# Performance work log

Hardware: AMD Instinct MI355X
Metric: run time of the kernel (lower is better)

The kernel has to match this reference:

```python
import jax, jax.numpy as jnp
import numpy as np

N = 50000   # nodes
E = 800000  # edges
F = 16      # raw feature width (sliced 4:10 -> 6)
H = 256     # hidden_dim
O = 128     # out_dim
NE = 4      # n_experts
G = 64      # graphs in batch
K = 2       # top_k
XS, XE = 4, 10
SPS = 0.3   # size_prior_strength


def setup_inputs() -> dict:
    key = jax.random.key(0)
    ks = jax.random.split(key, 16)
    rn = lambda k, s: jax.random.normal(k, s, dtype=jnp.float32) * 0.05
    return dict(
        x=jax.random.normal(ks[0], (N, F), dtype=jnp.float32),
        edge_index=jax.random.randint(ks[1], (2, E), 0, N),
        batch=jnp.sort(jax.random.randint(ks[2], (N,), 0, G)),
        enc_W1=rn(ks[3], (6, H)), enc_b1=jnp.zeros(H, jnp.float32),
        enc_W2=rn(ks[4], (H, H)), enc_b2=jnp.zeros(H, jnp.float32),
        r_W1=rn(ks[5], (H + 3, H)), r_b1=jnp.zeros(H, jnp.float32),
        ln_g=jnp.ones(H, jnp.float32), ln_b=jnp.zeros(H, jnp.float32),
        r_W2=rn(ks[6], (H, NE)), r_b2=jnp.zeros(NE, jnp.float32),
        size_centers=jnp.linspace(0.0, 1.0, NE, dtype=jnp.float32),
        W0_rel=rn(ks[7], (NE, H, H)), b0_rel=jnp.zeros((NE, H), jnp.float32), W0_root=rn(ks[8], (NE, H, H)),
        W1_rel=rn(ks[9], (NE, H, H)), b1_rel=jnp.zeros((NE, H), jnp.float32), W1_root=rn(ks[10], (NE, H, H)),
        W2_rel=rn(ks[11], (NE, H, O)), b2_rel=jnp.zeros((NE, O), jnp.float32), W2_root=rn(ks[12], (NE, H, O)),
    )


def _forward(x, edge_index, batch, enc_W1, enc_b1, enc_W2, enc_b2,
             r_W1, r_b1, ln_g, ln_b, r_W2, r_b2, size_centers,
             W0_rel, b0_rel, W0_root, W1_rel, b1_rel, W1_root, W2_rel, b2_rel, W2_root):
    src, dst = edge_index[0], edge_index[1]
    xs = x[:, XS:XE]                                   # [N,6]
    h = jax.nn.relu(xs @ enc_W1 + enc_b1) @ enc_W2 + enc_b2  # [N,H]

    # per-graph size features (bincounts via scatter-add)
    n = jnp.maximum(jnp.zeros(G, jnp.float32).at[batch].add(1.0), 1.0)
    e = jnp.zeros(G, jnp.float32).at[batch[src]].add(1.0)
    density = e / jnp.maximum(n * (n - 1.0), 1.0)
    logn = jnp.log(n)
    logn_norm = (logn - logn.min()) / (logn.max() - logn.min() + 1e-6)
    feats = jnp.stack([n, e, density], -1)             # [G,3]
    feats = (feats - feats.mean(0, keepdims=True)) / (feats.std(0, keepdims=True) + 1e-6)
    sf = feats[batch]                                   # [N,3]
    ln_node = logn_norm[batch]                          # [N]

    # router: Linear -> LayerNorm -> ReLU -> Linear, combined with size prior
    inp = jnp.concatenate([h, sf], -1)                  # [N,H+3]
    t = inp @ r_W1 + r_b1
    t = (t - t.mean(-1, keepdims=True)) * jax.lax.rsqrt(t.var(-1, keepdims=True) + 1e-5) * ln_g + ln_b
    learned = jax.nn.relu(t) @ r_W2 + r_b2              # [N,NE]
    prior = -(ln_node[:, None] - size_centers[None, :]) ** 2
    logits = (1.0 - SPS) * learned + SPS * prior        # temperature = 1.0

    # top-k gate
    probs = jax.nn.softmax(logits, -1)
    top_vals, top_idx = jax.lax.top_k(probs, K)
    top_vals = top_vals / (top_vals.sum(-1, keepdims=True) + 1e-8)
    weights = jnp.zeros_like(probs).at[jnp.arange(N)[:, None], top_idx].set(top_vals)

    # GraphConv experts: out = lin_rel(sum_{j->i} x_j) + lin_root(x_i)
    def aggregate(v):  # [N,C] -> [N,C] scatter-add of src features onto dst
        return jnp.zeros_like(v).at[dst].add(v[src])

    agg_h = aggregate(h)
    hE = jax.nn.relu(jnp.einsum('nh,eho->eno', agg_h, W0_rel) + b0_rel[:, None, :]
                     + jnp.einsum('nh,eho->eno', h, W0_root))            # [NE,N,H]
    aggE = jax.vmap(aggregate)(hE)
    hE = jax.nn.relu(jnp.einsum('enh,eho->eno', aggE, W1_rel) + b1_rel[:, None, :]
                     + jnp.einsum('enh,eho->eno', hE, W1_root))          # [NE,N,H]
    aggE = jax.vmap(aggregate)(hE)
    outE = (jnp.einsum('enh,eho->eno', aggE, W2_rel) + b2_rel[:, None, :]
            + jnp.einsum('enh,eho->eno', hE, W2_root))                   # [NE,N,O]

    return jnp.einsum('eno,ne->no', outE, weights)                       # [N,O]


def reference(x, edge_index, batch, enc_W1, enc_b1, enc_W2, enc_b2,
              r_W1, r_b1, ln_g, ln_b, r_W2, r_b2, size_centers,
              W0_rel, b0_rel, W0_root, W1_rel, b1_rel, W1_root, W2_rel, b2_rel, W2_root):
    return _forward(x, edge_index, batch, enc_W1, enc_b1, enc_W2, enc_b2,
                    r_W1, r_b1, ln_g, ln_b, r_W2, r_b2, size_centers,
                    W0_rel, b0_rel, W0_root, W1_rel, b1_rel, W1_root, W2_rel, b2_rel, W2_root)
```

## Files before the change

kernel.cpp:

```cpp
#include <hip/hip_runtime.h>
#include <hip/hip_bf16.h>

#define H_DIM 256
#define O_DIM 128
#define NEXP 4
#define G_DIM 64

typedef unsigned short ushort_t;
typedef unsigned int uint_t;
typedef __attribute__((ext_vector_type(8))) short short8;
typedef __attribute__((ext_vector_type(4))) float floatx4;

__device__ __forceinline__ float bf2f(ushort_t u) {
    union { uint_t i; float f; } c; c.i = ((uint_t)u) << 16; return c.f;
}
__device__ __forceinline__ ushort_t f2bf(float f) {
    union { float f; uint_t i; } c; c.f = f;
    uint_t x = c.i;
    uint_t r = (x + 0x7fffu + ((x >> 16) & 1u)) >> 16;
    return (ushort_t)r;
}

__device__ __forceinline__ void load16_lds(const void* g, void* l) {
    __builtin_amdgcn_global_load_lds(
        (const __attribute__((address_space(1))) unsigned int*)g,
        (__attribute__((address_space(3))) unsigned int*)l, 16, 0, 0);
}

__global__ void zero_i_kernel(int* __restrict__ p, long n) {
    long i = (long)blockIdx.x * blockDim.x + threadIdx.x;
    if (i < n) p[i] = 0;
}

__global__ void wsplit2_kernel(const float* __restrict__ Wa, const float* __restrict__ Wb,
                               ushort_t* __restrict__ Wh) {
    int z = blockIdx.y;
    int i = blockIdx.x * 256 + threadIdx.x;
    if (i >= 131072) return;
    int nn = i >> 9, kk = i & 511;
    float v = (kk < 256) ? Wa[(long)z * 65536 + kk * 256 + nn]
                         : Wb[(long)z * 65536 + (kk - 256) * 256 + nn];
    Wh[(long)z * 131072 + i] = f2bf(v);
}

__global__ void wsplitcat_kernel(const float* __restrict__ Wa, const float* __restrict__ Wb,
                                 ushort_t* __restrict__ Wh) {
    int z = blockIdx.y;
    int i = blockIdx.x * 256 + threadIdx.x;
    if (i >= 65536) return;
    int nn = i >> 8, kk = i & 255;
    float v = (nn < 128) ? Wa[(long)z * 32768 + kk * 128 + nn]
                         : Wb[(long)z * 32768 + kk * 128 + (nn - 128)];
    Wh[(long)z * 65536 + i] = f2bf(v);
}

__global__ void encoder1_kernel(const float* __restrict__ x, const float* __restrict__ W1,
                                const float* __restrict__ b1, float* __restrict__ u,
                                int N, int F) {
    int n = blockIdx.x;
    int j = threadIdx.x;
    float acc = b1[j];
    #pragma unroll
    for (int c = 0; c < 6; ++c)
        acc += x[(long)n * F + 4 + c] * W1[c * H_DIM + j];
    u[(long)n * H_DIM + j] = fmaxf(acc, 0.f);
}

__global__ __launch_bounds__(256)
void gemm256_kernel(const float* __restrict__ A, const float* __restrict__ W,
                    const float* __restrict__ bias, float* __restrict__ C,
                    ushort_t* __restrict__ Cbf, int M, int Nc) {
    const int K = 256;
    __shared__ float As[16][68];
    __shared__ float Ws[16][68];
    int tid = threadIdx.x;
    int tx = tid & 15, ty = tid >> 4;
    int row0 = blockIdx.x * 64;
    int col0 = blockIdx.y * 64;
    float acc[4][4] = {};
    int lrow = tid >> 2, kq = tid & 3;
    int wk = tid >> 4, wc = (tid & 15) * 4;
    for (int k0 = 0; k0 < K; k0 += 16) {
        float4 av = make_float4(0.f, 0.f, 0.f, 0.f);
        int arow = row0 + lrow;
        if (arow < M) av = *(const float4*)(A + (long)arow * K + k0 + kq * 4);
        As[kq * 4 + 0][lrow] = av.x;
        As[kq * 4 + 1][lrow] = av.y;
        As[kq * 4 + 2][lrow] = av.z;
        As[kq * 4 + 3][lrow] = av.w;
        float4 wv = *(const float4*)(W + (long)(k0 + wk) * Nc + col0 + wc);
        *(float4*)&Ws[wk][wc] = wv;
        __syncthreads();
        #pragma unroll
        for (int kk = 0; kk < 16; ++kk) {
            float a[4], b[4];
            #pragma unroll
            for (int i = 0; i < 4; ++i) a[i] = As[kk][ty * 4 + i];
            #pragma unroll
            for (int j = 0; j < 4; ++j) b[j] = Ws[kk][tx * 4 + j];
            #pragma unroll
            for (int i = 0; i < 4; ++i)
                #pragma unroll
                for (int j = 0; j < 4; ++j) acc[i][j] += a[i] * b[j];
        }
        __syncthreads();
    }
    #pragma unroll
    for (int i = 0; i < 4; ++i) {
        int r = row0 + ty * 4 + i;
        if (r >= M) break;
        #pragma unroll
        for (int j = 0; j < 4; ++j) {
            int c = col0 + tx * 4 + j;
            float v = acc[i][j];
            if (bias) v += bias[c];
            C[(long)r * Nc + c] = v;
            if (Cbf) Cbf[(long)r * Nc + c] = f2bf(v);
        }
    }
}

template<int NH>
__global__ __launch_bounds__(256)
void gemm_bf_kernel(const ushort_t* __restrict__ A1, long sA1z, int rsA1,
                    const ushort_t* __restrict__ A2, long sA2z, int rsA2,
                    const ushort_t* __restrict__ B, long sBz,
                    const float* __restrict__ bias, int sBiasz,
                    ushort_t* __restrict__ Cbf, long sCz, int rsC,
                    int M, int Kb, int relu) {
    __shared__ alignas(16) ushort_t Asl[2][64 * 32];
    __shared__ alignas(16) ushort_t Bsl[2][128 * 32];

    const int tid = threadIdx.x, wave = tid >> 6, lane = tid & 63;
    const int z = blockIdx.z;
    const int row0 = blockIdx.x * 64, col0 = blockIdx.y * 128;
    const int wr = (wave >> 1) * 32, wcx = (wave & 1) * 64;
    floatx4 acc[2][4] = {};

    A1 += (long)z * sA1z;
    A2 += (long)z * sA2z;
    B += (long)z * sBz;
    if (bias) bias += (long)z * sBiasz;
    Cbf += (long)z * sCz;

    const int bsr = lane >> 2;
    const int bgc = ((lane & 3) - (bsr >> 1)) & 3;
    long aoff1, aoff2;
    {
        int ar = row0 + wave * 16 + bsr;
        ar = ar < M ? ar : M - 1;
        aoff1 = (long)ar * rsA1 + bgc * 8;
        aoff2 = (long)ar * rsA2 + bgc * 8;
    }
    const long brow = (long)(col0 + wave * 32 + bsr) * Kb + bgc * 8;
    const ushort_t* Bg0 = B + brow;
    const ushort_t* Bg1 = B + brow + (long)16 * Kb;
    const int laA  = (wave * 16) * 32;
    const int laB0 = (wave * 32) * 32;
    const int laB1 = (wave * 32 + 16) * 32;

    const int fm = lane & 15, fq = lane >> 4;
    const int NK = NH * 8;

    load16_lds(A1 + aoff1, &Asl[0][laA]);
    load16_lds(Bg0, &Bsl[0][laB0]);
    load16_lds(Bg1, &Bsl[0][laB1]);
    __syncthreads();

    for (int k = 0; k < NK; ++k) {
        const int buf = k & 1;
        short8 a[2], b[4];
        #pragma unroll
        for (int j = 0; j < 4; ++j) {
            int row = wcx + j * 16 + fm;
            int slot = (fq + ((row >> 1) & 3)) & 3;
            b[j] = *(const short8*)&Bsl[buf][row * 32 + slot * 8];
        }
        #pragma unroll
        for (int i = 0; i < 2; ++i) {
            int row = wr + i * 16 + fm;
            int slot = (fq + ((row >> 1) & 3)) & 3;
            a[i] = *(const short8*)&Asl[buf][row * 32 + slot * 8];
        }
        if (k + 1 < NK) {
            const int kn = k + 1, bn = kn & 1;
            const ushort_t* Ab = (kn >> 3) ? A2 : A1;
            const long ao = (kn >> 3) ? aoff2 : aoff1;
            const int k0 = (kn & 7) * 32;
            const int kk = kn * 32;
            load16_lds(Ab + ao + k0, &Asl[bn][laA]);
            load16_lds(Bg0 + kk, &Bsl[bn][laB0]);
            load16_lds(Bg1 + kk, &Bsl[bn][laB1]);
        }
        #pragma unroll
        for (int i = 0; i < 2; ++i)
            #pragma unroll
            for (int j = 0; j < 4; ++j)
                acc[i][j] = __builtin_amdgcn_mfma_f32_16x16x32_bf16(a[i], b[j], acc[i][j], 0, 0, 0);
        if (k + 1 < NK) __syncthreads();
    }

    #pragma unroll
    for (int i = 0; i < 2; ++i) {
        #pragma unroll
        for (int j = 0; j < 4; ++j) {
            int col = col0 + wcx + j * 16 + fm;
            int rowb = row0 + wr + i * 16 + fq * 4;
            #pragma unroll
            for (int r = 0; r < 4; ++r) {
                int row = rowb + r;
                if (row < M) {
                    float v = acc[i][j][r];
                    if (bias) v += bias[col];
                    if (relu) v = fmaxf(v, 0.f);
                    Cbf[(long)row * rsC + col] = f2bf(v);
                }
            }
        }
    }
}

__global__ void hist_nodes_kernel(const int* __restrict__ batch, int n, int* __restrict__ gn) {
    __shared__ int bins[G_DIM];
    int t = threadIdx.x;
    if (t < G_DIM) bins[t] = 0;
    __syncthreads();
    for (long i = (long)blockIdx.x * blockDim.x + t; i < n; i += (long)gridDim.x * blockDim.x)
        atomicAdd(&bins[batch[i]], 1);
    __syncthreads();
    if (t < G_DIM) atomicAdd(&gn[t], bins[t]);
}

__global__ void hist_edges_kernel(const int* __restrict__ ei, const int* __restrict__ batch,
                                  int E, int* __restrict__ ge) {
    __shared__ int bins[G_DIM];
    int t = threadIdx.x;
    if (t < G_DIM) bins[t] = 0;
    __syncthreads();
    for (long i = (long)blockIdx.x * blockDim.x + t; i < E; i += (long)gridDim.x * blockDim.x)
        atomicAdd(&bins[batch[ei[i]]], 1);
    __syncthreads();
    if (t < G_DIM) atomicAdd(&ge[t], bins[t]);
}

__global__ void graph_stats_kernel(const int* __restrict__ gn, const int* __restrict__ ge,
                                   float* __restrict__ feats_norm, float* __restrict__ logn_norm) {
    int g = threadIdx.x;
    float nv = fmaxf((float)gn[g], 1.0f);
    float ev = (float)ge[g];
    float density = ev / fmaxf(nv * (nv - 1.0f), 1.0f);
    float logn = logf(nv);
    float mn = logn, mx = logn;
    for (int o = 32; o; o >>= 1) {
        mn = fminf(mn, __shfl_xor(mn, o));
        mx = fmaxf(mx, __shfl_xor(mx, o));
    }
    logn_norm[g] = (logn - mn) / (mx - mn + 1e-6f);
    float f[3] = {nv, ev, density};
    #pragma unroll
    for (int c = 0; c < 3; ++c) {
        float s = f[c];
        for (int o = 32; o; o >>= 1) s += __shfl_xor(s, o);
        float mean = s / 64.f;
        float d = f[c] - mean;
        float v = d * d;
        for (int o = 32; o; o >>= 1) v += __shfl_xor(v, o);
        float stdv = sqrtf(v / 64.f);
        feats_norm[g * 3 + c] = d / (stdv + 1e-6f);
    }
}

__global__ __launch_bounds__(256)
void router_epi_kernel(const float* __restrict__ t, const int* __restrict__ batch,
                       const float* __restrict__ feats_norm, const float* __restrict__ logn_norm,
                       const float* __restrict__ rW1, const float* __restrict__ rb1,
                       const float* __restrict__ lng, const float* __restrict__ lnb,
                       const float* __restrict__ rW2, const float* __restrict__ rb2,
                       const float* __restrict__ centers, float* __restrict__ w, int N) {
    int wave = threadIdx.x >> 6, lane = threadIdx.x & 63;
    int n = blockIdx.x * 4 + wave;
    if (n >= N) return;
    int g = batch[n];
    float sf0 = feats_norm[g * 3 + 0], sf1 = feats_norm[g * 3 + 1], sf2 = feats_norm[g * 3 + 2];
    float ln = logn_norm[g];
    float tv[4];
    #pragma unroll
    for (int q = 0; q < 4; ++q) {
        int j = lane + 64 * q;
        tv[q] = t[(long)n * H_DIM + j] + rb1[j]
              + sf0 * rW1[256 * H_DIM + j] + sf1 * rW1[257 * H_DIM + j] + sf2 * rW1[258 * H_DIM + j];
    }
    float s = tv[0] + tv[1] + tv[2] + tv[3];
    for (int o = 32; o; o >>= 1) s += __shfl_xor(s, o);
    float mean = s / 256.f;
    float vs = 0.f;
    #pragma unroll
    for (int q = 0; q < 4; ++q) { float d = tv[q] - mean; vs += d * d; }
    for (int o = 32; o; o >>= 1) vs += __shfl_xor(vs, o);
    float rstd = rsqrtf(vs / 256.f + 1e-5f);
    float le[NEXP] = {0.f, 0.f, 0.f, 0.f};
    #pragma unroll
    for (int q = 0; q < 4; ++q) {
        int j = lane + 64 * q;
        float y = (tv[q] - mean) * rstd * lng[j] + lnb[j];
        y = fmaxf(y, 0.f);
        #pragma unroll
        for (int e = 0; e < NEXP; ++e) le[e] += y * rW2[j * NEXP + e];
    }
    #pragma unroll
    for (int e = 0; e < NEXP; ++e)
        for (int o = 32; o; o >>= 1) le[e] += __shfl_xor(le[e], o);
    if (lane == 0) {
        float p[NEXP];
        float m = -1e30f;
        #pragma unroll
        for (int e = 0; e < NEXP; ++e) {
            float d = ln - centers[e];
            float lv = 0.7f * (le[e] + rb2[e]) + 0.3f * (-(d * d));
            p[e] = lv;
            m = fmaxf(m, lv);
        }
        float ssum = 0.f;
        #pragma unroll
        for (int e = 0; e < NEXP; ++e) { p[e] = expf(p[e] - m); ssum += p[e]; }
        #pragma unroll
        for (int e = 0; e < NEXP; ++e) p[e] /= ssum;
        int i1 = 0;
        for (int e = 1; e < NEXP; ++e) if (p[e] > p[i1]) i1 = e;
        int i2 = -1;
        for (int e = 0; e < NEXP; ++e) { if (e == i1) continue; if (i2 < 0 || p[e] > p[i2]) i2 = e; }
        float denom = p[i1] + p[i2] + 1e-8f;
        float out4[NEXP] = {0.f, 0.f, 0.f, 0.f};
        out4[i1] = p[i1] / denom;
        out4[i2] = p[i2] / denom;
        #pragma unroll
        for (int e = 0; e < NEXP; ++e) w[(long)n * NEXP + e] = out4[e];
    }
}

__global__ void count_dst_kernel(const int* __restrict__ ei, int E, int* __restrict__ cnt) {
    int i = blockIdx.x * blockDim.x + threadIdx.x;
    if (i < E) atomicAdd(&cnt[ei[E + i]], 1);
}

__global__ __launch_bounds__(1024)
void scan_kernel(const int* __restrict__ cnt, int* __restrict__ row_ptr, int n) {
    __shared__ int buf[1024];
    __shared__ int carry_s;
    int tid = threadIdx.x;
    if (tid == 0) carry_s = 0;
    __syncthreads();
    for (int base = 0; base < n; base += 1024) {
        int v = (base + tid < n) ? cnt[base + tid] : 0;
        buf[tid] = v;
        __syncthreads();
        for (int off = 1; off < 1024; off <<= 1) {
            int tv = (tid >= off) ? buf[tid - off] : 0;
            __syncthreads();
            buf[tid] += tv;
            __syncthreads();
        }
        int carry = carry_s;
        if (base + tid < n) row_ptr[base + tid] = carry + buf[tid] - v;
        __syncthreads();
        if (tid == 1023) carry_s = carry + buf[1023];
        __syncthreads();
    }
    if (tid == 0) row_ptr[n] = carry_s;
}

__global__ void fill_csr_kernel(const int* __restrict__ ei, int E, const int* __restrict__ row_ptr,
                                int* __restrict__ fillc, int* __restrict__ srcs) {
    int i = blockIdx.x * blockDim.x + threadIdx.x;
    if (i < E) {
        int d = ei[E + i];
        int pos = row_ptr[d] + atomicAdd(&fillc[d], 1);
        srcs[pos] = ei[i];
    }
}

__global__ __launch_bounds__(256)
void agg_b2b_kernel(const ushort_t* __restrict__ feat, ushort_t* __restrict__ outp,
                    const int* __restrict__ rp, const int* __restrict__ srcs, int N) {
    int wave = threadIdx.x >> 6, lane = threadIdx.x & 63;
    int n = blockIdx.x * 4 + wave;
    if (n >= N) return;
    float a0 = 0.f, a1 = 0.f, a2 = 0.f, a3 = 0.f;
    int p0 = rp[n], p1 = rp[n + 1];
    const ushort_t* base = feat + lane * 4;
    int p = p0;
    for (; p + 3 < p1; p += 4) {
        uint2 v0 = *(const uint2*)(base + (long)srcs[p] * H_DIM);
        uint2 v1 = *(const uint2*)(base + (long)srcs[p + 1] * H_DIM);
        uint2 v2 = *(const uint2*)(base + (long)srcs[p + 2] * H_DIM);
        uint2 v3 = *(const uint2*)(base + (long)srcs[p + 3] * H_DIM);
        a0 += bf2f((ushort_t)(v0.x & 0xffff)) + bf2f((ushort_t)(v1.x & 0xffff))
            + bf2f((ushort_t)(v2.x & 0xffff)) + bf2f((ushort_t)(v3.x & 0xffff));
        a1 += bf2f((ushort_t)(v0.x >> 16)) + bf2f((ushort_t)(v1.x >> 16))
            + bf2f((ushort_t)(v2.x >> 16)) + bf2f((ushort_t)(v3.x >> 16));
        a2 += bf2f((ushort_t)(v0.y & 0xffff)) + bf2f((ushort_t)(v1.y & 0xffff))
            + bf2f((ushort_t)(v2.y & 0xffff)) + bf2f((ushort_t)(v3.y & 0xffff));
        a3 += bf2f((ushort_t)(v0.y >> 16)) + bf2f((ushort_t)(v1.y >> 16))
            + bf2f((ushort_t)(v2.y >> 16)) + bf2f((ushort_t)(v3.y >> 16));
    }
    for (; p < p1; ++p) {
        uint2 v = *(const uint2*)(base + (long)srcs[p] * H_DIM);
        a0 += bf2f((ushort_t)(v.x & 0xffff));
        a1 += bf2f((ushort_t)(v.x >> 16));
        a2 += bf2f((ushort_t)(v.y & 0xffff));
        a3 += bf2f((ushort_t)(v.y >> 16));
    }
    uint2 o;
    o.x = (uint_t)f2bf(a0) | ((uint_t)f2bf(a1) << 16);
    o.y = (uint_t)f2bf(a2) | ((uint_t)f2bf(a3) << 16);
    *(uint2*)(outp + (long)n * H_DIM + lane * 4) = o;
}

__global__ void aggI_kernel(const ushort_t* __restrict__ feat, ushort_t* __restrict__ outp,
                            const int* __restrict__ rp, const int* __restrict__ srcs,
                            int N, int W) {
    int n = blockIdx.x;
    int t = threadIdx.x;
    float a[8] = {0.f, 0.f, 0.f, 0.f, 0.f, 0.f, 0.f, 0.f};
    int p0 = rp[n], p1 = rp[n + 1];
    const ushort_t* base = feat + t * 8;
    int p = p0;
    for (; p + 3 < p1; p += 4) {
        uint4 v0 = *(const uint4*)(base + (long)srcs[p] * W);
        uint4 v1 = *(const uint4*)(base + (long)srcs[p + 1] * W);
        uint4 v2 = *(const uint4*)(base + (long)srcs[p + 2] * W);
        uint4 v3 = *(const uint4*)(base + (long)srcs[p + 3] * W);
        uint_t w0[4] = {v0.x, v0.y, v0.z, v0.w};
        uint_t w1[4] = {v1.x, v1.y, v1.z, v1.w};
        uint_t w2[4] = {v2.x, v2.y, v2.z, v2.w};
        uint_t w3[4] = {v3.x, v3.y, v3.z, v3.w};
        #pragma unroll
        for (int q = 0; q < 4; ++q) {
            a[2 * q]     += bf2f((ushort_t)(w0[q] & 0xffff)) + bf2f((ushort_t)(w1[q] & 0xffff))
                          + bf2f((ushort_t)(w2[q] & 0xffff)) + bf2f((ushort_t)(w3[q] & 0xffff));
            a[2 * q + 1] += bf2f((ushort_t)(w0[q] >> 16)) + bf2f((ushort_t)(w1[q] >> 16))
                          + bf2f((ushort_t)(w2[q] >> 16)) + bf2f((ushort_t)(w3[q] >> 16));
        }
    }
    for (; p < p1; ++p) {
        uint4 v = *(const uint4*)(base + (long)srcs[p] * W);
        uint_t w[4] = {v.x, v.y, v.z, v.w};
        #pragma unroll
        for (int q = 0; q < 4; ++q) {
            a[2 * q]     += bf2f((ushort_t)(w[q] & 0xffff));
            a[2 * q + 1] += bf2f((ushort_t)(w[q] >> 16));
        }
    }
    uint4 o;
    o.x = (uint_t)f2bf(a[0]) | ((uint_t)f2bf(a[1]) << 16);
    o.y = (uint_t)f2bf(a[2]) | ((uint_t)f2bf(a[3]) << 16);
    o.z = (uint_t)f2bf(a[4]) | ((uint_t)f2bf(a[5]) << 16);
    o.w = (uint_t)f2bf(a[6]) | ((uint_t)f2bf(a[7]) << 16);
    *(uint4*)(outp + (long)n * W + t * 8) = o;
}

__global__ __launch_bounds__(256)
void final_mixE_kernel(const ushort_t* __restrict__ PR, const float* __restrict__ b2,
                       const float* __restrict__ wts, int e0, int EB,
                       const int* __restrict__ rp, const int* __restrict__ srcs,
                       float* __restrict__ out, int N, int init) {
    int wave = threadIdx.x >> 6, lane = threadIdx.x & 63;
    int n = blockIdx.x * 4 + wave;
    if (n >= N) return;
    const int W = EB * 256;
    int c0 = lane * 2;
    long obase = (long)n * O_DIM + c0;
    float o0 = init ? 0.f : out[obase];
    float o1 = init ? 0.f : out[obase + 1];
    int zs[2]; float wv[2]; int na = 0;
    for (int z = 0; z < EB; ++z) {
        float w = wts[(long)n * NEXP + e0 + z];
        if (w != 0.f && na < 2) { zs[na] = z; wv[na] = w; ++na; }
    }
    if (na) {
        const ushort_t* P0 = PR + zs[0] * 256 + c0;
        const ushort_t* P1 = PR + zs[na - 1] * 256 + c0;
        float a00 = 0.f, a01 = 0.f, a10 = 0.f, a11 = 0.f;
        int p0 = rp[n], p1 = rp[n + 1];
        if (na == 2) {
            int p = p0;
            for (; p + 1 < p1; p += 2) {
                long s0 = (long)srcs[p] * W;
                long s1 = (long)srcs[p + 1] * W;
                uint_t v00 = *(const uint_t*)(P0 + s0);
                uint_t v10 = *(const uint_t*)(P1 + s0);
                uint_t v01 = *(const uint_t*)(P0 + s1);
                uint_t v11 = *(const uint_t*)(P1 + s1);
                a00 += bf2f((ushort_t)(v00 & 0xffff)) + bf2f((ushort_t)(v01 & 0xffff));
                a01 += bf2f((ushort_t)(v00 >> 16))    + bf2f((ushort_t)(v01 >> 16));
                a10 += bf2f((ushort_t)(v10 & 0xffff)) + bf2f((ushort_t)(v11 & 0xffff));
                a11 += bf2f((ushort_t)(v10 >> 16))    + bf2f((ushort_t)(v11 >> 16));
            }
            if (p < p1) {
                long s = (long)srcs[p] * W;
                uint_t v0 = *(const uint_t*)(P0 + s);
                uint_t v1 = *(const uint_t*)(P1 + s);
                a00 += bf2f((ushort_t)(v0 & 0xffff)); a01 += bf2f((ushort_t)(v0 >> 16));
                a10 += bf2f((ushort_t)(v1 & 0xffff)); a11 += bf2f((ushort_t)(v1 >> 16));
            }
        } else {
            int p = p0;
            for (; p + 3 < p1; p += 4) {
                uint_t v0 = *(const uint_t*)(P0 + (long)srcs[p] * W);
                uint_t v1 = *(const uint_t*)(P0 + (long)srcs[p + 1] * W);
                uint_t v2 = *(const uint_t*)(P0 + (long)srcs[p + 2] * W);
                uint_t v3 = *(const uint_t*)(P0 + (long)srcs[p + 3] * W);
                a00 += bf2f((ushort_t)(v0 & 0xffff)) + bf2f((ushort_t)(v1 & 0xffff))
                     + bf2f((ushort_t)(v2 & 0xffff)) + bf2f((ushort_t)(v3 & 0xffff));
                a01 += bf2f((ushort_t)(v0 >> 16)) + bf2f((ushort_t)(v1 >> 16))
                     + bf2f((ushort_t)(v2 >> 16)) + bf2f((ushort_t)(v3 >> 16));
            }
            for (; p < p1; ++p) {
                uint_t v = *(const uint_t*)(P0 + (long)srcs[p] * W);
                a00 += bf2f((ushort_t)(v & 0xffff)); a01 += bf2f((ushort_t)(v >> 16));
            }
        }
        {
            int e = e0 + zs[0];
            uint_t rv = *(const uint_t*)(PR + (long)n * W + zs[0] * 256 + 128 + c0);
            o0 += wv[0] * (a00 + bf2f((ushort_t)(rv & 0xffff)) + b2[e * O_DIM + c0]);
            o1 += wv[0] * (a01 + bf2f((ushort_t)(rv >> 16))    + b2[e * O_DIM + c0 + 1]);
        }
        if (na == 2) {
            int e = e0 + zs[1];
            uint_t rv = *(const uint_t*)(PR + (long)n * W + zs[1] * 256 + 128 + c0);
            o0 += wv[1] * (a10 + bf2f((ushort_t)(rv & 0xffff)) + b2[e * O_DIM + c0]);
            o1 += wv[1] * (a11 + bf2f((ushort_t)(rv >> 16))    + b2[e * O_DIM + c0 + 1]);
        }
    }
    out[obase] = o0;
    out[obase + 1] = o1;
}

extern "C" void kernel_launch(void* const* d_in, const int* in_sizes, int n_in,
                              void* d_out, int out_size, void* d_ws, size_t ws_size,
                              hipStream_t stream) {
    const float* x       = (const float*)d_in[0];
    const int*   ei      = (const int*)  d_in[1];
    const int*   batch   = (const int*)  d_in[2];
    const float* enc_W1  = (const float*)d_in[3];
    const float* enc_b1  = (const float*)d_in[4];
    const float* enc_W2  = (const float*)d_in[5];
    const float* enc_b2  = (const float*)d_in[6];
    const float* r_W1    = (const float*)d_in[7];
    const float* r_b1    = (const float*)d_in[8];
    const float* ln_g    = (const float*)d_in[9];
    const float* ln_b    = (const float*)d_in[10];
    const float* r_W2    = (const float*)d_in[11];
    const float* r_b2    = (const float*)d_in[12];
    const float* centers = (const float*)d_in[13];
    const float* W0_rel  = (const float*)d_in[14];
    const float* b0_rel  = (const float*)d_in[15];
    const float* W0_root = (const float*)d_in[16];
    const float* W1_rel  = (const float*)d_in[17];
    const float* b1_rel  = (const float*)d_in[18];
    const float* W1_root = (const float*)d_in[19];
    const float* W2_rel  = (const float*)d_in[20];
    const float* b2_rel  = (const float*)d_in[21];
    const float* W2_root = (const float*)d_in[22];

    const int N = in_sizes[2];
    const int E = in_sizes[1] / 2;
    const int F = in_sizes[0] / N;

    char* ws = (char*)d_ws;
    size_t off = 0;
    auto alloc = [&](size_t bytes) -> void* {
        void* p = ws + off;
        off += (bytes + 255) & ~(size_t)255;
        return p;
    };
    int* cnt      = (int*)alloc((size_t)N * 4);
    int* fillc    = (int*)alloc((size_t)N * 4);
    int* gn       = (int*)alloc((size_t)G_DIM * 4);
    int* ge       = (int*)alloc((size_t)G_DIM * 4);
    size_t zero_bytes = off;
    int* row_ptr  = (int*)alloc((size_t)(N + 1) * 4);
    int* srcs     = (int*)alloc((size_t)E * 4);
    float* feats_norm = (float*)alloc((size_t)G_DIM * 3 * 4);
    float* logn_norm  = (float*)alloc((size_t)G_DIM * 4);
    float* wts    = (float*)alloc((size_t)N * NEXP * 4);
    ushort_t* wf0  = (ushort_t*)alloc((size_t)NEXP * 131072 * 2);
    ushort_t* wf1  = (ushort_t*)alloc((size_t)NEXP * 131072 * 2);
    ushort_t* wfin = (ushort_t*)alloc((size_t)NEXP * 65536 * 2);

    const long sE = (long)N * H_DIM;
    size_t fixed_end = off;
    size_t slab4 = ((size_t)4 * sE * 2 + 255) & ~(size_t)255;
    size_t slab2 = ((size_t)2 * sE * 2 + 255) & ~(size_t)255;
    size_t need4 = fixed_end + 3 * slab4 + (1u << 20);

    int EB;
    ushort_t *S1, *S2, *S3, *h_bf, *aggh_bf;
    float *u, *h, *tf32;
    if (ws_size >= need4) {
        EB = 4;
        S1 = (ushort_t*)alloc(slab4);
        S2 = (ushort_t*)alloc(slab4);
        S3 = (ushort_t*)alloc(slab4);
        u = (float*)S1; h = (float*)S2;
        h_bf = S3; aggh_bf = S3 + sE;
        tf32 = (float*)(S3 + 2 * sE);
    } else {
        EB = 2;
        h_bf    = (ushort_t*)alloc((size_t)sE * 2);
        aggh_bf = (ushort_t*)alloc((size_t)sE * 2);
        S1 = (ushort_t*)alloc(slab2);
        S2 = (ushort_t*)alloc(slab2);
        S3 = (ushort_t*)alloc(slab2);
        u = (float*)S1; h = (float*)S2; tf32 = (float*)S3;
    }
    (void)out_size; (void)n_in;

    ushort_t* hE0  = S1;
    ushort_t* aggE = S2;
    ushort_t* hE1  = S3;
    ushort_t* PR   = S1;
    float* out = (float*)d_out;

    const int W  = EB * 256;
    dim3 blk256(256);
    dim3 gR((N + 63) / 64, H_DIM / 64, 1);
    dim3 gM((N + 63) / 64, 2, EB);
    dim3 gAgg((N + 3) / 4);

    {
        long nz = (long)(zero_bytes / 4);
        zero_i_kernel<<<dim3((nz + 255) / 256), blk256, 0, stream>>>((int*)ws, nz);
    }
    wsplit2_kernel<<<dim3(512, NEXP), blk256, 0, stream>>>(W0_rel, W0_root, wf0);
    wsplit2_kernel<<<dim3(512, NEXP), blk256, 0, stream>>>(W1_rel, W1_root, wf1);
    wsplitcat_kernel<<<dim3(256, NEXP), blk256, 0, stream>>>(W2_rel, W2_root, wfin);
    encoder1_kernel<<<dim3(N), blk256, 0, stream>>>(x, enc_W1, enc_b1, u, N, F);
    gemm256_kernel<<<gR, blk256, 0, stream>>>(u, enc_W2, enc_b2, h, h_bf, N, H_DIM);
    hist_nodes_kernel<<<dim3(256), blk256, 0, stream>>>(batch, N, gn);
    hist_edges_kernel<<<dim3(512), blk256, 0, stream>>>(ei, batch, E, ge);
    graph_stats_kernel<<<dim3(1), dim3(64), 0, stream>>>(gn, ge, feats_norm, logn_norm);
    gemm256_kernel<<<gR, blk256, 0, stream>>>(h, r_W1, nullptr, tf32, nullptr, N, H_DIM);
    router_epi_kernel<<<dim3((N + 3) / 4), blk256, 0, stream>>>(
        tf32, batch, feats_norm, logn_norm, r_W1, r_b1, ln_g, ln_b, r_W2, r_b2, centers, wts, N);
    count_dst_kernel<<<dim3((E + 255) / 256), blk256, 0, stream>>>(ei, E, cnt);
    scan_kernel<<<dim3(1), dim3(1024), 0, stream>>>(cnt, row_ptr, N);
    fill_csr_kernel<<<dim3((E + 255) / 256), blk256, 0, stream>>>(ei, E, row_ptr, fillc, srcs);
    agg_b2b_kernel<<<gAgg, blk256, 0, stream>>>(h_bf, aggh_bf, row_ptr, srcs, N);

    for (int b = 0; b < NEXP / EB; ++b) {
        const int e0 = b * EB;
        gemm_bf_kernel<2><<<gM, blk256, 0, stream>>>(
            aggh_bf, 0, 256, h_bf, 0, 256,
            wf0 + (long)e0 * 131072, 131072,
            b0_rel + e0 * H_DIM, H_DIM, hE0, 256, W, N, 512, 1);
        aggI_kernel<<<dim3(N), dim3(W / 8), 0, stream>>>(hE0, aggE, row_ptr, srcs, N, W);
        gemm_bf_kernel<2><<<gM, blk256, 0, stream>>>(
            aggE, 256, W, hE0, 256, W,
            wf1 + (long)e0 * 131072, 131072,
            b1_rel + e0 * H_DIM, H_DIM, hE1, 256, W, N, 512, 1);
        gemm_bf_kernel<1><<<gM, blk256, 0, stream>>>(
            hE1, 256, W, nullptr, 0, 256,
            wfin + (long)e0 * 65536, 65536,
            nullptr, 0, PR, 256, W, N, 256, 0);
        final_mixE_kernel<<<gAgg, blk256, 0, stream>>>(
            PR, b2_rel, wts, e0, EB, row_ptr, srcs, out, N, b == 0 ? 1 : 0);
    }
}
```

Measured before the change: 1.252 ms.

## Slice expert aggregation by 64-byte column chunks for L2 locality

Replaces the per-node aggregation kernel, which read full W-wide rows with uint4 loads, with a sliced variant. Each block covers 16 nodes and one 32-column slice, and block IDs are interleaved so that 8 slices of the same node group run together. The aim is to shrink the working set touched by the random neighbour gathers at any moment, so more of it stays in L2/MALL. The cost is narrower 4-byte loads per lane and more index reads, since each edge index is now loaded once per slice.

```diff
diff --git a/kernel.cpp b/kernel.cpp
--- a/kernel.cpp
+++ b/kernel.cpp
@@ -416,47 +416,39 @@
     *(uint2*)(outp + (long)n * H_DIM + lane * 4) = o;
 }
 
-__global__ void aggI_kernel(const ushort_t* __restrict__ feat, ushort_t* __restrict__ outp,
-                            const int* __restrict__ rp, const int* __restrict__ srcs,
-                            int N, int W) {
-    int n = blockIdx.x;
-    int t = threadIdx.x;
-    float a[8] = {0.f, 0.f, 0.f, 0.f, 0.f, 0.f, 0.f, 0.f};
+__global__ __launch_bounds__(256)
+void aggSlice_kernel(const ushort_t* __restrict__ feat, ushort_t* __restrict__ outp,
+                     const int* __restrict__ rp, const int* __restrict__ srcs,
+                     int N, int W, int NB) {
+    int bid = blockIdx.x;
+    int x = bid & 7, g = bid >> 3;
+    int s = x + 8 * (g / NB);
+    int ng = g % NB;
+    int wave = threadIdx.x >> 6, lane = threadIdx.x & 63;
+    int q = lane >> 4, l = lane & 15;
+    int n = ng * 16 + wave * 4 + q;
+    if (n >= N) return;
+    const ushort_t* base = feat + s * 32 + l * 2;
     int p0 = rp[n], p1 = rp[n + 1];
-    const ushort_t* base = feat + t * 8;
+    float a0 = 0.f, a1 = 0.f;
     int p = p0;
     for (; p + 3 < p1; p += 4) {
-        uint4 v0 = *(const uint4*)(base + (long)srcs[p] * W);
-        uint4 v1 = *(const uint4*)(base + (long)srcs[p + 1] * W);
-        uint4 v2 = *(const uint4*)(base + (long)srcs[p + 2] * W);
-        uint4 v3 = *(const uint4*)(base + (long)srcs[p + 3] * W);
-        uint_t w0[4] = {v0.x, v0.y, v0.z, v0.w};
-        uint_t w1[4] = {v1.x, v1.y, v1.z, v1.w};
-        uint_t w2[4] = {v2.x, v2.y, v2.z, v2.w};
-        uint_t w3[4] = {v3.x, v3.y, v3.z, v3.w};
-        #pragma unroll
-        for (int q = 0; q < 4; ++q) {
-            a[2 * q]     += bf2f((ushort_t)(w0[q] & 0xffff)) + bf2f((ushort_t)(w1[q] & 0xffff))
-                          + bf2f((ushort_t)(w2[q] & 0xffff)) + bf2f((ushort_t)(w3[q] & 0xffff));
-            a[2 * q + 1] += bf2f((ushort_t)(w0[q] >> 16)) + bf2f((ushort_t)(w1[q] >> 16))
-                          + bf2f((ushort_t)(w2[q] >> 16)) + bf2f((ushort_t)(w3[q] >> 16));
-        }
+        uint_t u0 = *(const uint_t*)(base + (long)srcs[p] * W);
+        uint_t u1 = *(const uint_t*)(base + (long)srcs[p + 1] * W);
+        uint_t u2 = *(const uint_t*)(base + (long)srcs[p + 2] * W);
+        uint_t u3 = *(const uint_t*)(base + (long)srcs[p + 3] * W);
+        a0 += bf2f((ushort_t)(u0 & 0xffff)) + bf2f((ushort_t)(u1 & 0xffff))
+            + bf2f((ushort_t)(u2 & 0xffff)) + bf2f((ushort_t)(u3 & 0xffff));
+        a1 += bf2f((ushort_t)(u0 >> 16)) + bf2f((ushort_t)(u1 >> 16))
+            + bf2f((ushort_t)(u2 >> 16)) + bf2f((ushort_t)(u3 >> 16));
     }
     for (; p < p1; ++p) {
-        uint4 v = *(const uint4*)(base + (long)srcs[p] * W);
-        uint_t w[4] = {v.x, v.y, v.z, v.w};
-        #pragma unroll
-        for (int q = 0; q < 4; ++q) {
-            a[2 * q]     += bf2f((ushort_t)(w[q] & 0xffff));
-            a[2 * q + 1] += bf2f((ushort_t)(w[q] >> 16));
-        }
-    }
-    uint4 o;
-    o.x = (uint_t)f2bf(a[0]) | ((uint_t)f2bf(a[1]) << 16);
-    o.y = (uint_t)f2bf(a[2]) | ((uint_t)f2bf(a[3]) << 16);
-    o.z = (uint_t)f2bf(a[4]) | ((uint_t)f2bf(a[5]) << 16);
-    o.w = (uint_t)f2bf(a[6]) | ((uint_t)f2bf(a[7]) << 16);
-    *(uint4*)(outp + (long)n * W + t * 8) = o;
+        uint_t u = *(const uint_t*)(base + (long)srcs[p] * W);
+        a0 += bf2f((ushort_t)(u & 0xffff));
+        a1 += bf2f((ushort_t)(u >> 16));
+    }
+    uint_t o = (uint_t)f2bf(a0) | ((uint_t)f2bf(a1) << 16);
+    *(uint_t*)(outp + (long)n * W + s * 32 + l * 2) = o;
 }
 
 __global__ __launch_bounds__(256)
@@ -628,6 +620,8 @@
     dim3 gR((N + 63) / 64, H_DIM / 64, 1);
     dim3 gM((N + 63) / 64, 2, EB);
     dim3 gAgg((N + 3) / 4);
+    const int NB = (N + 15) / 16;
+    const int PS = W / 32;
 
     {
         long nz = (long)(zero_bytes / 4);
@@ -655,7 +649,7 @@
             aggh_bf, 0, 256, h_bf, 0, 256,
             wf0 + (long)e0 * 131072, 131072,
             b0_rel + e0 * H_DIM, H_DIM, hE0, 256, W, N, 512, 1);
-        aggI_kernel<<<dim3(N), dim3(W / 8), 0, stream>>>(hE0, aggE, row_ptr, srcs, N, W);
+        aggSlice_kernel<<<dim3(NB * PS), blk256, 0, stream>>>(hE0, aggE, row_ptr, srcs, N, W, NB);
         gemm_bf_kernel<2><<<gM, blk256, 0, stream>>>(
             aggE, 256, W, hE0, 256, W,
             wf1 + (long)e0 * 131072, 131072,
```

Measured after the change: 1.374 ms. 1.1x slower.

## Fuse neighbor aggregation into layer-1 expert GEMM A-tile staging

Applied to the files above, without the earlier changes.

Removes the separate aggI kernel and its intermediate aggE buffer. The new GEMM gathers and sums neighbor rows directly into the LDS A tile for the first half of K (the aggregated part), then loads the root features for the second half. Each block now covers the full 256 output columns, so every gathered row is used once, instead of writing and rereading aggE. The cost is that the irregular gather now sits inside the GEMM main loop and can stall the MFMA pipeline. Grid parallelism also drops by half.

```diff
diff --git a/kernel.cpp b/kernel.cpp
--- a/kernel.cpp
+++ b/kernel.cpp
@@ -220,6 +220,176 @@
     }
 }
 
+__global__ __launch_bounds__(256)
+void gemm_ag_kernel(const ushort_t* __restrict__ F, int zoff,
+                    const ushort_t* __restrict__ B, long sBz,
+                    const float* __restrict__ bias, int sBiasz,
+                    ushort_t* __restrict__ Cbf, long sCz, int rsC,
+                    const int* __restrict__ rp, const int* __restrict__ srcs,
+                    int M, int W, int Kb) {
+    __shared__ alignas(16) ushort_t Asl[2][64 * 32];
+    __shared__ alignas(16) ushort_t Bsl[2][256 * 32];
+
+    const int tid = threadIdx.x, wave = tid >> 6, lane = tid & 63;
+    const int z = blockIdx.z;
+    const int row0 = blockIdx.x * 64;
+    const int wr = (wave >> 1) * 32, wcx = (wave & 1) * 128;
+    floatx4 acc[2][8] = {};
+
+    const ushort_t* Fz = F + (long)z * zoff;
+    B += (long)z * sBz;
+    bias += (long)z * sBiasz;
+    Cbf += (long)z * sCz;
+
+    const int bsr = lane >> 2;
+    const int bgc = ((lane & 3) - (bsr >> 1)) & 3;
+    int ar = row0 + wave * 16 + bsr;
+    ar = ar < M ? ar : M - 1;
+    const int ap0 = rp[ar], ap1 = rp[ar + 1];
+    const ushort_t* gb0  = Fz + bgc * 8;
+    const ushort_t* aptr = Fz + (long)ar * W + bgc * 8;
+
+    const long brow = (long)(wave * 64 + bsr) * Kb + bgc * 8;
+    const ushort_t* Bg = B + brow;
+    const int laA = (wave * 16) * 32;
+    const int laB = (wave * 64) * 32;
+    const int fm = lane & 15, fq = lane >> 4;
+
+    auto bstage = [&](int kk, int buf) {
+        const int ko = kk * 32;
+        load16_lds(Bg + ko,                 &Bsl[buf][laB]);
+        load16_lds(Bg + ko + (long)16 * Kb, &Bsl[buf][laB + 16 * 32]);
+        load16_lds(Bg + ko + (long)32 * Kb, &Bsl[buf][laB + 32 * 32]);
+        load16_lds(Bg + ko + (long)48 * Kb, &Bsl[buf][laB + 48 * 32]);
+    };
+    auto gstage = [&](int kk, int buf) {
+        const ushort_t* gb = gb0 + kk * 32;
+        float a[8] = {0.f, 0.f, 0.f, 0.f, 0.f, 0.f, 0.f, 0.f};
+        int p = ap0;
+        for (; p + 7 < ap1; p += 8) {
+            uint4 v0 = *(const uint4*)(gb + (long)srcs[p] * W);
+            uint4 v1 = *(const uint4*)(gb + (long)srcs[p + 1] * W);
+            uint4 v2 = *(const uint4*)(gb + (long)srcs[p + 2] * W);
+            uint4 v3 = *(const uint4*)(gb + (long)srcs[p + 3] * W);
+            uint4 v4 = *(const uint4*)(gb + (long)srcs[p + 4] * W);
+            uint4 v5 = *(const uint4*)(gb + (long)srcs[p + 5] * W);
+            uint4 v6 = *(const uint4*)(gb + (long)srcs[p + 6] * W);
+            uint4 v7 = *(const uint4*)(gb + (long)srcs[p + 7] * W);
+            {
+                uint_t w0[4] = {v0.x, v0.y, v0.z, v0.w};
+                uint_t w1[4] = {v1.x, v1.y, v1.z, v1.w};
+                uint_t w2[4] = {v2.x, v2.y, v2.z, v2.w};
+                uint_t w3[4] = {v3.x, v3.y, v3.z, v3.w};
+                #pragma unroll
+                for (int q = 0; q < 4; ++q) {
+                    a[2 * q]     += bf2f((ushort_t)(w0[q] & 0xffff)) + bf2f((ushort_t)(w1[q] & 0xffff))
+                                  + bf2f((ushort_t)(w2[q] & 0xffff)) + bf2f((ushort_t)(w3[q] & 0xffff));
+                    a[2 * q + 1] += bf2f((ushort_t)(w0[q] >> 16)) + bf2f((ushort_t)(w1[q] >> 16))
+                                  + bf2f((ushort_t)(w2[q] >> 16)) + bf2f((ushort_t)(w3[q] >> 16));
+                }
+            }
+            {
+                uint_t w0[4] = {v4.x, v4.y, v4.z, v4.w};
+                uint_t w1[4] = {v5.x, v5.y, v5.z, v5.w};
+                uint_t w2[4] = {v6.x, v6.y, v6.z, v6.w};
+                uint_t w3[4] = {v7.x, v7.y, v7.z, v7.w};
+                #pragma unroll
+                for (int q = 0; q < 4; ++q) {
+                    a[2 * q]     += bf2f((ushort_t)(w0[q] & 0xffff)) + bf2f((ushort_t)(w1[q] & 0xffff))
+                                  + bf2f((ushort_t)(w2[q] & 0xffff)) + bf2f((ushort_t)(w3[q] & 0xffff));
+                    a[2 * q + 1] += bf2f((ushort_t)(w0[q] >> 16)) + bf2f((ushort_t)(w1[q] >> 16))
+                                  + bf2f((ushort_t)(w2[q] >> 16)) + bf2f((ushort_t)(w3[q] >> 16));
+                }
+            }
+        }
+        for (; p + 3 < ap1; p += 4) {
+            uint4 v0 = *(const uint4*)(gb + (long)srcs[p] * W);
+            uint4 v1 = *(const uint4*)(gb + (long)srcs[p + 1] * W);
+            uint4 v2 = *(const uint4*)(gb + (long)srcs[p + 2] * W);
+            uint4 v3 = *(const uint4*)(gb + (long)srcs[p + 3] * W);
+            uint_t w0[4] = {v0.x, v0.y, v0.z, v0.w};
+            uint_t w1[4] = {v1.x, v1.y, v1.z, v1.w};
+            uint_t w2[4] = {v2.x, v2.y, v2.z, v2.w};
+            uint_t w3[4] = {v3.x, v3.y, v3.z, v3.w};
+            #pragma unroll
+            for (int q = 0; q < 4; ++q) {
+                a[2 * q]     += bf2f((ushort_t)(w0[q] & 0xffff)) + bf2f((ushort_t)(w1[q] & 0xffff))
+                              + bf2f((ushort_t)(w2[q] & 0xffff)) + bf2f((ushort_t)(w3[q] & 0xffff));
+                a[2 * q + 1] += bf2f((ushort_t)(w0[q] >> 16)) + bf2f((ushort_t)(w1[q] >> 16))
+                              + bf2f((ushort_t)(w2[q] >> 16)) + bf2f((ushort_t)(w3[q] >> 16));
+            }
+        }
+        for (; p < ap1; ++p) {
+            uint4 v = *(const uint4*)(gb + (long)srcs[p] * W);
+            uint_t w[4] = {v.x, v.y, v.z, v.w};
+            #pragma unroll
+            for (int q = 0; q < 4; ++q) {
+                a[2 * q]     += bf2f((ushort_t)(w[q] & 0xffff));
+                a[2 * q + 1] += bf2f((ushort_t)(w[q] >> 16));
+            }
+        }
+        uint4 o;
+        o.x = (uint_t)f2bf(a[0]) | ((uint_t)f2bf(a[1]) << 16);
+        o.y = (uint_t)f2bf(a[2]) | ((uint_t)f2bf(a[3]) << 16);
+        o.z = (uint_t)f2bf(a[4]) | ((uint_t)f2bf(a[5]) << 16);
+        o.w = (uint_t)f2bf(a[6]) | ((uint_t)f2bf(a[7]) << 16);
+        *(uint4*)&Asl[buf][laA + lane * 8] = o;
+    };
+
+    bstage(0, 0);
+    gstage(0, 0);
+    __syncthreads();
+
+    for (int k = 0; k < 16; ++k) {
+        const int buf = k & 1;
+        short8 af[2], b[8];
+        #pragma unroll
+        for (int j = 0; j < 8; ++j) {
+            int row = wcx + j * 16 + fm;
+            int slot = (fq + ((row >> 1) & 3)) & 3;
+            b[j] = *(const short8*)&Bsl[buf][row * 32 + slot * 8];
+        }
+        #pragma unroll
+        for (int i = 0; i < 2; ++i) {
+            int row = wr + i * 16 + fm;
+            int slot = (fq + ((row >> 1) & 3)) & 3;
+            af[i] = *(const short8*)&Asl[buf][row * 32 + slot * 8];
+        }
+        const int kn = k + 1, bn = kn & 1;
+        if (kn < 16) {
+            bstage(kn, bn);
+            if (kn >= 8) load16_lds(aptr + (kn - 8) * 32, &Asl[bn][laA]);
+        }
+        #pragma unroll
+        for (int i = 0; i < 2; ++i)
+            #pragma unroll
+            for (int j = 0; j < 8; ++j)
+                acc[i][j] = __builtin_amdgcn_mfma_f32_16x16x32_bf16(af[i], b[j], acc[i][j], 0, 0, 0);
+        if (kn < 16) {
+            if (kn < 8) gstage(kn, bn);
+            __syncthreads();
+        }
+    }
+
+    #pragma unroll
+    for (int i = 0; i < 2; ++i) {
+        #pragma unroll
+        for (int j = 0; j < 8; ++j) {
+            int col = wcx + j * 16 + fm;
+            int rowb = row0 + wr + i * 16 + fq * 4;
+            #pragma unroll
+            for (int r = 0; r < 4; ++r) {
+                int row = rowb + r;
+                if (row < M) {
+                    float v = acc[i][j][r] + bias[col];
+                    v = fmaxf(v, 0.f);
+                    Cbf[(long)row * rsC + col] = f2bf(v);
+                }
+            }
+        }
+    }
+}
+
 __global__ void hist_nodes_kernel(const int* __restrict__ batch, int n, int* __restrict__ gn) {
     __shared__ int bins[G_DIM];
     int t = threadIdx.x;
@@ -414,49 +584,6 @@
     o.x = (uint_t)f2bf(a0) | ((uint_t)f2bf(a1) << 16);
     o.y = (uint_t)f2bf(a2) | ((uint_t)f2bf(a3) << 16);
     *(uint2*)(outp + (long)n * H_DIM + lane * 4) = o;
-}
-
-__global__ void aggI_kernel(const ushort_t* __restrict__ feat, ushort_t* __restrict__ outp,
-                            const int* __restrict__ rp, const int* __restrict__ srcs,
-                            int N, int W) {
-    int n = blockIdx.x;
-    int t = threadIdx.x;
-    float a[8] = {0.f, 0.f, 0.f, 0.f, 0.f, 0.f, 0.f, 0.f};
-    int p0 = rp[n], p1 = rp[n + 1];
-    const ushort_t* base = feat + t * 8;
-    int p = p0;
-    for (; p + 3 < p1; p += 4) {
-        uint4 v0 = *(const uint4*)(base + (long)srcs[p] * W);
-        uint4 v1 = *(const uint4*)(base + (long)srcs[p + 1] * W);
-        uint4 v2 = *(const uint4*)(base + (long)srcs[p + 2] * W);
-        uint4 v3 = *(const uint4*)(base + (long)srcs[p + 3] * W);
-        uint_t w0[4] = {v0.x, v0.y, v0.z, v0.w};
-        uint_t w1[4] = {v1.x, v1.y, v1.z, v1.w};
-        uint_t w2[4] = {v2.x, v2.y, v2.z, v2.w};
-        uint_t w3[4] = {v3.x, v3.y, v3.z, v3.w};
-        #pragma unroll
-        for (int q = 0; q < 4; ++q) {
-            a[2 * q]     += bf2f((ushort_t)(w0[q] & 0xffff)) + bf2f((ushort_t)(w1[q] & 0xffff))
-                          + bf2f((ushort_t)(w2[q] & 0xffff)) + bf2f((ushort_t)(w3[q] & 0xffff));
-            a[2 * q + 1] += bf2f((ushort_t)(w0[q] >> 16)) + bf2f((ushort_t)(w1[q] >> 16))
-                          + bf2f((ushort_t)(w2[q] >> 16)) + bf2f((ushort_t)(w3[q] >> 16));
-        }
-    }
-    for (; p < p1; ++p) {
-        uint4 v = *(const uint4*)(base + (long)srcs[p] * W);
-        uint_t w[4] = {v.x, v.y, v.z, v.w};
-        #pragma unroll
-        for (int q = 0; q < 4; ++q) {
-            a[2 * q]     += bf2f((ushort_t)(w[q] & 0xffff));
-            a[2 * q + 1] += bf2f((ushort_t)(w[q] >> 16));
-        }
-    }
-    uint4 o;
-    o.x = (uint_t)f2bf(a[0]) | ((uint_t)f2bf(a[1]) << 16);
-    o.y = (uint_t)f2bf(a[2]) | ((uint_t)f2bf(a[3]) << 16);
-    o.z = (uint_t)f2bf(a[4]) | ((uint_t)f2bf(a[5]) << 16);
-    o.w = (uint_t)f2bf(a[6]) | ((uint_t)f2bf(a[7]) << 16);
-    *(uint4*)(outp + (long)n * W + t * 8) = o;
 }
 
 __global__ __launch_bounds__(256)
@@ -618,7 +745,6 @@
     (void)out_size; (void)n_in;
 
     ushort_t* hE0  = S1;
-    ushort_t* aggE = S2;
     ushort_t* hE1  = S3;
     ushort_t* PR   = S1;
     float* out = (float*)d_out;
@@ -627,6 +753,7 @@
     dim3 blk256(256);
     dim3 gR((N + 63) / 64, H_DIM / 64, 1);
     dim3 gM((N + 63) / 64, 2, EB);
+    dim3 gA((N + 63) / 64, 1, EB);
     dim3 gAgg((N + 3) / 4);
 
     {
@@ -655,11 +782,12 @@
             aggh_bf, 0, 256, h_bf, 0, 256,
             wf0 + (long)e0 * 131072, 131072,
             b0_rel + e0 * H_DIM, H_DIM, hE0, 256, W, N, 512, 1);
-        aggI_kernel<<<dim3(N), dim3(W / 8), 0, stream>>>(hE0, aggE, row_ptr, srcs, N, W);
-        gemm_bf_kernel<2><<<gM, blk256, 0, stream>>>(
-            aggE, 256, W, hE0, 256, W,
+        gemm_ag_kernel<<<gA, blk256, 0, stream>>>(
+            hE0, 256,
             wf1 + (long)e0 * 131072, 131072,
-            b1_rel + e0 * H_DIM, H_DIM, hE1, 256, W, N, 512, 1);
+            b1_rel + e0 * H_DIM, H_DIM,
+            hE1, 256, W,
+            row_ptr, srcs, N, W, 512);
         gemm_bf_kernel<1><<<gM, blk256, 0, stream>>>(
             hE1, 256, W, nullptr, 0, 256,
             wfin + (long)e0 * 65536, 65536,
```

After: 1.351 ms. +7.9%, slower.
